# Kernel tuning notes

Hardware: AMD Instinct MI355X
Metric: run time of the kernel (lower is better)

## Reference

```python
import jax, jax.numpy as jnp
import numpy as np
from jax import lax

NEG = -1e30  # log-space 'zero' (avoid -inf for mixed-precision safety)
EPS = 1e-7   # keras backend epsilon used in ctc_batch_cost


def setup_inputs() -> dict:
    key = jax.random.key(0)
    k1, k2 = jax.random.split(key)
    B, T, L, V = 64, 1024, 128, 512
    # labels in [0, V-2]; blank index is V-1 (keras ctc_batch_cost convention)
    y_true = jax.random.randint(k1, (B, L), 0, V - 1, dtype=jnp.int64)
    # y_pred are softmax probabilities (ctc_batch_cost logs them internally)
    y_pred = jax.random.uniform(k2, (B, T, V), dtype=jnp.float32)
    y_pred = y_pred / jnp.sum(y_pred, axis=-1, keepdims=True)
    return {"y_true": y_true, "y_pred": y_pred}


def _ctc_loss(y_true, y_pred):
    # y_true: [B, L] int labels; y_pred: [B, T, V] probabilities
    B, T, V = y_pred.shape
    L = y_true.shape[1]
    blank = V - 1
    S = 2 * L + 1  # extended label length: blank,l1,blank,l2,...,blank

    logp = jnp.log(y_pred + EPS)  # [B, T, V]

    # extended label sequence per batch row
    ext = jnp.full((B, S), blank, dtype=y_true.dtype)
    ext = ext.at[:, 1::2].set(y_true)  # [B, S]

    # gather log-probs of extended labels at every time step -> [B, T, S]
    idx = jnp.broadcast_to(ext[:, None, :], (B, T, S))
    lp = jnp.take_along_axis(logp, idx, axis=2)

    # skip transition s-2 -> s allowed iff ext[s] != blank and ext[s] != ext[s-2]
    prev2 = jnp.concatenate([jnp.full((B, 2), -1, dtype=ext.dtype), ext[:, :-2]], axis=1)
    allow_skip = (ext != blank) & (ext != prev2)  # [B, S]

    # init alpha at t=0: only states 0 (blank) and 1 (first label) reachable
    alpha0 = jnp.full((B, S), NEG, dtype=logp.dtype)
    alpha0 = alpha0.at[:, 0].set(lp[:, 0, 0]).at[:, 1].set(lp[:, 0, 1])

    pad1 = jnp.full((B, 1), NEG, dtype=logp.dtype)
    pad2 = jnp.full((B, 2), NEG, dtype=logp.dtype)

    def step(alpha, lp_t):  # alpha, lp_t: [B, S]
        a1 = jnp.concatenate([pad1, alpha[:, :-1]], axis=1)
        a2 = jnp.concatenate([pad2, alpha[:, :-2]], axis=1)
        a2 = jnp.where(allow_skip, a2, NEG)
        new = jnp.logaddexp(jnp.logaddexp(alpha, a1), a2) + lp_t
        return new, None

    lp_rest = jnp.moveaxis(lp[:, 1:], 1, 0)  # [T-1, B, S], time-major for scan
    alpha_T, _ = lax.scan(step, alpha0, lp_rest)

    # total prob ends in last blank or last label
    log_p = jnp.logaddexp(alpha_T[:, -1], alpha_T[:, -2])  # [B]
    return -log_p[:, None]  # [B, 1] like keras ctc_batch_cost


def reference(y_true, y_pred):
    return _ctc_loss(y_true, y_pred)
```

## Files before the change

### kernel.cpp

```cpp
#include <hip/hip_runtime.h>
#include <hip/hip_bf16.h>
#include <cstdint>


#define CTC_B 64
#define CTC_T 1024
#define CTC_L 128
#define CTC_V 512
#define BLANK (CTC_V - 1)
#define EPSF 1e-7f
#define LN2F 0.69314718055994530942f

#define CHUNK 16
#define NBUF  4
#define NCH   (CTC_T / CHUNK)
#define BIASE 60

__device__ __forceinline__ void gld_lds16(const float* g, float* l) {
    __builtin_amdgcn_global_load_lds(
        (const __attribute__((address_space(1))) unsigned int*)g,
        (__attribute__((address_space(3))) unsigned int*)l,
        16, 0, 0);
}

template<int CTRL>
__device__ __forceinline__ float dpp_mov0(float v) {
    int r = __builtin_amdgcn_update_dpp(0, __float_as_int(v), CTRL, 0xf, 0xf, false);
    return __int_as_float(r);
}
template<int CTRL>
__device__ __forceinline__ float dpp_max(float v) {
    int r = __builtin_amdgcn_update_dpp(__float_as_int(v), __float_as_int(v),
                                        CTRL, 0xf, 0xf, false);
    return fmaxf(v, __int_as_float(r));
}

__global__ __launch_bounds__(256, 1)
void ctc_fwd_stream(const int* __restrict__ y_true,
                    const float* __restrict__ y_pred,
                    float* __restrict__ out) {
    __shared__ __align__(16) float rows[NBUF][CHUNK][CTC_V];

    const int b = blockIdx.x;
    const int tid = threadIdx.x;
    const int wave = tid >> 6;
    const int lane = tid & 63;
    const float* __restrict__ yb = y_pred + (size_t)b * CTC_T * CTC_V;

    if (wave != 0) {
        const int w = wave - 1;
#define ISSUE(c_) do {                                                     \
            const int t0_ = (c_) * CHUNK;                                  \
            float* bufb_ = &rows[(c_) & (NBUF - 1)][0][0];                 \
            for (int l_ = w; l_ < CHUNK; l_ += 3) {                        \
                const float* g_ = yb + (size_t)(t0_ + l_) * CTC_V + lane * 4; \
                float* d_ = bufb_ + l_ * CTC_V;                            \
                gld_lds16(g_, d_);                                         \
                gld_lds16(g_ + 256, d_ + 256);                             \
            }                                                              \
        } while (0)

        ISSUE(0); ISSUE(1); ISSUE(2);
        if (w == 0) asm volatile("s_waitcnt vmcnt(24)" ::: "memory");
        else        asm volatile("s_waitcnt vmcnt(20)" ::: "memory");
        __builtin_amdgcn_s_barrier();
        __builtin_amdgcn_sched_barrier(0);

        for (int c = 0; c < NCH; ++c) {
            if (c + 3 < NCH) ISSUE(c + 3);
            if (c <= NCH - 4) {
                if (w == 0) asm volatile("s_waitcnt vmcnt(24)" ::: "memory");
                else        asm volatile("s_waitcnt vmcnt(20)" ::: "memory");
            } else if (c == NCH - 3) {
                if (w == 0) asm volatile("s_waitcnt vmcnt(12)" ::: "memory");
                else        asm volatile("s_waitcnt vmcnt(10)" ::: "memory");
            } else if (c == NCH - 2) {
                asm volatile("s_waitcnt vmcnt(0)" ::: "memory");
            }
            __builtin_amdgcn_s_barrier();
            __builtin_amdgcn_sched_barrier(0);
        }
        return;
#undef ISSUE
    }

    const int labA = y_true[b * CTC_L + 2 * lane];
    const int labB = y_true[b * CTC_L + 2 * lane + 1];
    const int labPrev = __shfl_up(labB, 1);
    const float msk1 = (labA != labPrev) ? 1.0f : 0.0f;
    const float msk3 = (labB != labA) ? 1.0f : 0.0f;

    float a0 = 0.0f, a1 = 0.0f, a2 = 0.0f, a3 = 0.0f, a4 = 0.0f;
    float curScale = 1.0f;
    int curE = 0, Eacc = 0;

    float pAA0, pBA0, blA0, pAA1, pBA1, blA1, pAA2, pBA2, blA2, pAA3, pBA3, blA3;
    float pAB0, pBB0, blB0, pAB1, pBB1, blB1, pAB2, pBB2, blB2, pAB3, pBB3, blB3;
    float pAC0, pBC0, blC0, pAC1, pBC1, blC1, pAC2, pBC2, blC2, pAC3, pBC3, blC3;

#define LOADG(S, l_) do {                                                  \
        const float* r0_ = bufc + ((l_) + 0) * CTC_V;                      \
        const float* r1_ = bufc + ((l_) + 1) * CTC_V;                      \
        const float* r2_ = bufc + ((l_) + 2) * CTC_V;                      \
        const float* r3_ = bufc + ((l_) + 3) * CTC_V;                      \
        pA##S##0 = r0_[labA]; pB##S##0 = r0_[labB]; bl##S##0 = r0_[BLANK]; \
        pA##S##1 = r1_[labA]; pB##S##1 = r1_[labB]; bl##S##1 = r1_[BLANK]; \
        pA##S##2 = r2_[labA]; pB##S##2 = r2_[labB]; bl##S##2 = r2_[BLANK]; \
        pA##S##3 = r3_[labA]; pB##S##3 = r3_[labB]; bl##S##3 = r3_[BLANK]; \
    } while (0)

#define DOSTEP(S, k) do {                                                  \
        const float pb_ = bl##S##k + EPSF;                                 \
        const float pA_ = pA##S##k + EPSF;                                 \
        const float pB_ = pB##S##k + EPSF;                                 \
        const float pm1_ = dpp_mov0<0x138>(a3);  \
        const float n0_ = (a0 + pm1_) * pb_;                               \
        const float n1_ = fmaf(msk1, pm1_, a0 + a1) * pA_;                 \
        const float n2_ = (a1 + a2) * pb_;                                 \
        const float n3_ = fmaf(msk3, a1, a2 + a3) * pB_;                   \
        const float n4_ = (a3 + a4) * pb_;                                 \
        a0 = n0_; a1 = n1_; a2 = n2_; a3 = n3_; a4 = n4_;                  \
    } while (0)

#define DORN() do {                                                        \
        a0 *= curScale; a1 *= curScale; a2 *= curScale;                    \
        a3 *= curScale; a4 *= curScale;                                    \
        Eacc += curE;                                                      \
        float m_ = fmaxf(fmaxf(fmaxf(a0, a1), fmaxf(a2, a3)), a4);         \
        m_ = dpp_max<0x111>(m_);                           \
        m_ = dpp_max<0x112>(m_);                           \
        m_ = dpp_max<0x114>(m_);                           \
        m_ = dpp_max<0x118>(m_);                           \
        m_ = dpp_max<0x142>(m_);                         \
        m_ = dpp_max<0x143>(m_);                         \
        const int mb_ = __builtin_amdgcn_readlane(__float_as_int(m_), 63); \
        const int e_ = (mb_ >> 23) & 255;                                  \
        int k_ = 127 + BIASE + 127 - e_;                                   \
        k_ = k_ > 254 ? 254 : (k_ < 1 ? 1 : k_);                           \
        curScale = __int_as_float((unsigned)k_ << 23);                     \
        curE = 127 - k_;                                                   \
    } while (0)

#define PROC4_RN(S) do {                                                   \
        DOSTEP(S, 0); DORN();                                              \
        DOSTEP(S, 1); DOSTEP(S, 2); DOSTEP(S, 3);                          \
    } while (0)

    __builtin_amdgcn_s_barrier();
    __builtin_amdgcn_sched_barrier(0);

    for (int c = 0; c < NCH; ++c) {
        const float* bufc = &rows[c & (NBUF - 1)][0][0];
        if (c == 0) {
            const float pb0 = bufc[BLANK] + EPSF;
            const float plA = bufc[labA] + EPSF;
            LOADG(A, 0); LOADG(B, 4); LOADG(C, 8);
            a0 = (lane == 0) ? pb0 : 0.0f;
            a1 = (lane == 0) ? plA : 0.0f;
            DOSTEP(A, 1); DOSTEP(A, 2); DOSTEP(A, 3);
            LOADG(A, 12);
            PROC4_RN(B);
            PROC4_RN(C);
            PROC4_RN(A);
        } else {
            LOADG(A, 0); LOADG(B, 4); LOADG(C, 8);
            PROC4_RN(A); LOADG(A, 12);
            PROC4_RN(B); PROC4_RN(C); PROC4_RN(A);
        }
        __builtin_amdgcn_s_barrier();
        __builtin_amdgcn_sched_barrier(0);
    }

    if (lane == 63) {
        out[b] = -(logf(a3 + a4) + (float)Eacc * LN2F);
    }

#undef PROC4_RN
#undef DORN
#undef DOSTEP
#undef LOADG
}

extern "C" void kernel_launch(void* const* d_in, const int* in_sizes, int n_in,
                              void* d_out, int out_size, void* d_ws, size_t ws_size,
                              hipStream_t stream) {
    (void)in_sizes; (void)n_in; (void)d_ws; (void)ws_size; (void)out_size;
    const int* y_true = (const int*)d_in[0];
    const float* y_pred = (const float*)d_in[1];
    float* out = (float*)d_out;

    ctc_fwd_stream<<<CTC_B, 256, 0, stream>>>(y_true, y_pred, out);
}
```

Baseline: 71.42 us.

## Split CTC into parallel bf16 gather kernel plus compact serial scan kernel

Adds a gather kernel launched over 4096 blocks that reads the full probability tensor with all CUs. For each time step it keeps only the label and blank probabilities, packed as bf16 into a compact workspace of 68 words per row. A second kernel, one block per batch row, then runs the serial alpha recursion, streaming this small buffer through a deeper 8-slot LDS ring with a single loader wave. The goal is to lift the bandwidth limit of streaming the whole vocabulary through only 64 blocks, at the cost of an extra launch and bf16 rounding of the probabilities. The original single-kernel path is kept as a fallback when the workspace is too small.

```diff
diff --git a/kernel.cpp b/kernel.cpp
--- a/kernel.cpp
+++ b/kernel.cpp
@@ -11,16 +11,27 @@
 #define EPSF 1e-7f
 #define LN2F 0.69314718055994530942f
 
+#define ROWW 68
+#define K1ROWS 16
 #define CHUNK 16
-#define NBUF  4
+#define NBUF  8
 #define NCH   (CTC_T / CHUNK)
 #define BIASE 60
 
-__device__ __forceinline__ void gld_lds16(const float* g, float* l) {
+__device__ __forceinline__ void gld_lds16(const uint32_t* g, uint32_t* l) {
     __builtin_amdgcn_global_load_lds(
         (const __attribute__((address_space(1))) unsigned int*)g,
-        (__attribute__((address_space(3))) unsigned int*)l,
-        16, 0, 0);
+        (__attribute__((address_space(3))) unsigned int*)l, 16, 0, 0);
+}
+__device__ __forceinline__ void gld_lds4(const uint32_t* g, uint32_t* l) {
+    __builtin_amdgcn_global_load_lds(
+        (const __attribute__((address_space(1))) unsigned int*)g,
+        (__attribute__((address_space(3))) unsigned int*)l, 4, 0, 0);
+}
+__device__ __forceinline__ void gld_lds16f(const float* g, float* l) {
+    __builtin_amdgcn_global_load_lds(
+        (const __attribute__((address_space(1))) unsigned int*)g,
+        (__attribute__((address_space(3))) unsigned int*)l, 16, 0, 0);
 }
 
 template<int CTRL>
@@ -35,48 +46,81 @@
     return fmaxf(v, __int_as_float(r));
 }
 
+__device__ __forceinline__ uint32_t rne16(float x) {
+    return (__float_as_uint(x) + 0x8000u) >> 16;
+}
+
 __global__ __launch_bounds__(256, 1)
-void ctc_fwd_stream(const int* __restrict__ y_true,
-                    const float* __restrict__ y_pred,
-                    float* __restrict__ out) {
-    __shared__ __align__(16) float rows[NBUF][CHUNK][CTC_V];
+void ctc_gather(const int* __restrict__ y_true,
+                const float* __restrict__ y_pred,
+                uint32_t* __restrict__ cmp) {
+    __shared__ __align__(16) float rows[K1ROWS][CTC_V];
+
+    const int bid = blockIdx.x;
+    const int b = bid >> 6;
+    const int t0 = (bid & 63) * K1ROWS;
+    const int w = threadIdx.x >> 6;
+    const int lane = threadIdx.x & 63;
+    const float* __restrict__ yb = y_pred + ((size_t)b * CTC_T + t0) * CTC_V;
+
+    const int2 lp = *(const int2*)&y_true[b * CTC_L + 2 * lane];
+
+#pragma unroll
+    for (int r = 0; r < 4; ++r) {
+        const int row = 4 * w + r;
+        const float* g = yb + (size_t)row * CTC_V + lane * 4;
+        gld_lds16f(g, &rows[row][0]);
+        gld_lds16f(g + 256, &rows[row][256]);
+    }
+    asm volatile("s_waitcnt vmcnt(0)" ::: "memory");
+
+#pragma unroll
+    for (int r = 0; r < 4; ++r) {
+        const int row = 4 * w + r;
+        const float* rowp = &rows[row][0];
+        const float c0 = rowp[lp.x];
+        const float c1 = rowp[lp.y];
+        const uint32_t pk = rne16(c0) | (rne16(c1) << 16);
+        uint32_t* od = cmp + ((size_t)b * CTC_T + t0 + row) * ROWW;
+        od[lane] = pk;
+        if (lane == 63) od[64] = rne16(rowp[BLANK]);
+    }
+}
+
+__global__ __launch_bounds__(128, 1)
+void ctc_scan(const int* __restrict__ y_true,
+              const uint32_t* __restrict__ cmp,
+              float* __restrict__ out) {
+    __shared__ __align__(16) uint32_t ring[NBUF][CHUNK][ROWW];
 
     const int b = blockIdx.x;
-    const int tid = threadIdx.x;
-    const int wave = tid >> 6;
-    const int lane = tid & 63;
-    const float* __restrict__ yb = y_pred + (size_t)b * CTC_T * CTC_V;
-
-    if (wave != 0) {
-        const int w = wave - 1;
+    const int wave = threadIdx.x >> 6;
+    const int lane = threadIdx.x & 63;
+    const uint32_t* __restrict__ cb = cmp + (size_t)b * CTC_T * ROWW;
+
+    if (wave == 1) {
 #define ISSUE(c_) do {                                                     \
-            const int t0_ = (c_) * CHUNK;                                  \
-            float* bufb_ = &rows[(c_) & (NBUF - 1)][0][0];                 \
-            for (int l_ = w; l_ < CHUNK; l_ += 3) {                        \
-                const float* g_ = yb + (size_t)(t0_ + l_) * CTC_V + lane * 4; \
-                float* d_ = bufb_ + l_ * CTC_V;                            \
-                gld_lds16(g_, d_);                                         \
-                gld_lds16(g_ + 256, d_ + 256);                             \
-            }                                                              \
+            const uint32_t* g_ = cb + (size_t)(c_) * (CHUNK * ROWW);       \
+            uint32_t* d_ = &ring[(c_) & (NBUF - 1)][0][0];                 \
+            gld_lds16(g_ + lane * 4,        d_);                           \
+            gld_lds16(g_ + 256 + lane * 4,  d_ + 256);                     \
+            gld_lds16(g_ + 512 + lane * 4,  d_ + 512);                     \
+            gld_lds16(g_ + 768 + lane * 4,  d_ + 768);                     \
+            gld_lds4 (g_ + 1024 + lane,     d_ + 1024);                    \
         } while (0)
-
-        ISSUE(0); ISSUE(1); ISSUE(2);
-        if (w == 0) asm volatile("s_waitcnt vmcnt(24)" ::: "memory");
-        else        asm volatile("s_waitcnt vmcnt(20)" ::: "memory");
+        ISSUE(0); ISSUE(1); ISSUE(2); ISSUE(3); ISSUE(4); ISSUE(5);
+        asm volatile("s_waitcnt vmcnt(25)" ::: "memory");
         __builtin_amdgcn_s_barrier();
         __builtin_amdgcn_sched_barrier(0);
-
         for (int c = 0; c < NCH; ++c) {
-            if (c + 3 < NCH) ISSUE(c + 3);
-            if (c <= NCH - 4) {
-                if (w == 0) asm volatile("s_waitcnt vmcnt(24)" ::: "memory");
-                else        asm volatile("s_waitcnt vmcnt(20)" ::: "memory");
-            } else if (c == NCH - 3) {
-                if (w == 0) asm volatile("s_waitcnt vmcnt(12)" ::: "memory");
-                else        asm volatile("s_waitcnt vmcnt(10)" ::: "memory");
-            } else if (c == NCH - 2) {
-                asm volatile("s_waitcnt vmcnt(0)" ::: "memory");
-            }
+            if (c + 6 < NCH) ISSUE(c + 6);
+            const int K = (NCH - 1 - c < 6) ? (NCH - 1 - c) : 6;
+            if (K == 6)      asm volatile("s_waitcnt vmcnt(25)" ::: "memory");
+            else if (K == 5) asm volatile("s_waitcnt vmcnt(20)" ::: "memory");
+            else if (K == 4) asm volatile("s_waitcnt vmcnt(15)" ::: "memory");
+            else if (K == 3) asm volatile("s_waitcnt vmcnt(10)" ::: "memory");
+            else if (K == 2) asm volatile("s_waitcnt vmcnt(5)"  ::: "memory");
+            else if (K == 1) asm volatile("s_waitcnt vmcnt(0)"  ::: "memory");
             __builtin_amdgcn_s_barrier();
             __builtin_amdgcn_sched_barrier(0);
         }
@@ -94,25 +138,25 @@
     float curScale = 1.0f;
     int curE = 0, Eacc = 0;
 
-    float pAA0, pBA0, blA0, pAA1, pBA1, blA1, pAA2, pBA2, blA2, pAA3, pBA3, blA3;
-    float pAB0, pBB0, blB0, pAB1, pBB1, blB1, pAB2, pBB2, blB2, pAB3, pBB3, blB3;
-    float pAC0, pBC0, blC0, pAC1, pBC1, blC1, pAC2, pBC2, blC2, pAC3, pBC3, blC3;
+    uint32_t vA0, vA1, vA2, vA3, bA0, bA1, bA2, bA3;
+    uint32_t vB0, vB1, vB2, vB3, bB0, bB1, bB2, bB3;
+    uint32_t vC0, vC1, vC2, vC3, bC0, bC1, bC2, bC3;
 
 #define LOADG(S, l_) do {                                                  \
-        const float* r0_ = bufc + ((l_) + 0) * CTC_V;                      \
-        const float* r1_ = bufc + ((l_) + 1) * CTC_V;                      \
-        const float* r2_ = bufc + ((l_) + 2) * CTC_V;                      \
-        const float* r3_ = bufc + ((l_) + 3) * CTC_V;                      \
-        pA##S##0 = r0_[labA]; pB##S##0 = r0_[labB]; bl##S##0 = r0_[BLANK]; \
-        pA##S##1 = r1_[labA]; pB##S##1 = r1_[labB]; bl##S##1 = r1_[BLANK]; \
-        pA##S##2 = r2_[labA]; pB##S##2 = r2_[labB]; bl##S##2 = r2_[BLANK]; \
-        pA##S##3 = r3_[labA]; pB##S##3 = r3_[labB]; bl##S##3 = r3_[BLANK]; \
+        const uint32_t* r0_ = bufc + ((l_) + 0) * ROWW;                    \
+        const uint32_t* r1_ = bufc + ((l_) + 1) * ROWW;                    \
+        const uint32_t* r2_ = bufc + ((l_) + 2) * ROWW;                    \
+        const uint32_t* r3_ = bufc + ((l_) + 3) * ROWW;                    \
+        v##S##0 = r0_[lane]; b##S##0 = r0_[64];                            \
+        v##S##1 = r1_[lane]; b##S##1 = r1_[64];                            \
+        v##S##2 = r2_[lane]; b##S##2 = r2_[64];                            \
+        v##S##3 = r3_[lane]; b##S##3 = r3_[64];                            \
     } while (0)
 
 #define DOSTEP(S, k) do {                                                  \
-        const float pb_ = bl##S##k + EPSF;                                 \
-        const float pA_ = pA##S##k + EPSF;                                 \
-        const float pB_ = pB##S##k + EPSF;                                 \
+        const float pb_ = __uint_as_float(b##S##k << 16) + EPSF;           \
+        const float pA_ = __uint_as_float(v##S##k << 16) + EPSF;           \
+        const float pB_ = __uint_as_float(v##S##k & 0xffff0000u) + EPSF;   \
         const float pm1_ = dpp_mov0<0x138>(a3);  \
         const float n0_ = (a0 + pm1_) * pb_;                               \
         const float n1_ = fmaf(msk1, pm1_, a0 + a1) * pA_;                 \
@@ -150,13 +194,15 @@
     __builtin_amdgcn_sched_barrier(0);
 
     for (int c = 0; c < NCH; ++c) {
-        const float* bufc = &rows[c & (NBUF - 1)][0][0];
+        const uint32_t* bufc = &ring[c & (NBUF - 1)][0][0];
         if (c == 0) {
-            const float pb0 = bufc[BLANK] + EPSF;
-            const float plA = bufc[labA] + EPSF;
+            const uint32_t u0 = bufc[0];
+            const uint32_t ub0 = bufc[64];
             LOADG(A, 0); LOADG(B, 4); LOADG(C, 8);
+            const float pb0 = __uint_as_float(ub0 << 16) + EPSF;
+            const float pl0 = __uint_as_float(u0 << 16) + EPSF;
             a0 = (lane == 0) ? pb0 : 0.0f;
-            a1 = (lane == 0) ? plA : 0.0f;
+            a1 = (lane == 0) ? pl0 : 0.0f;
             DOSTEP(A, 1); DOSTEP(A, 2); DOSTEP(A, 3);
             LOADG(A, 12);
             PROC4_RN(B);
@@ -174,20 +220,161 @@
     if (lane == 63) {
         out[b] = -(logf(a3 + a4) + (float)Eacc * LN2F);
     }
-
 #undef PROC4_RN
 #undef DORN
 #undef DOSTEP
 #undef LOADG
 }
 
+#define F_CHUNK 16
+#define F_NBUF  4
+#define F_NCH   (CTC_T / F_CHUNK)
+
+__global__ __launch_bounds__(256, 1)
+void ctc_fwd_stream(const int* __restrict__ y_true,
+                    const float* __restrict__ y_pred,
+                    float* __restrict__ out) {
+    __shared__ __align__(16) float rows[F_NBUF][F_CHUNK][CTC_V];
+    const int b = blockIdx.x;
+    const int tid = threadIdx.x;
+    const int wave = tid >> 6;
+    const int lane = tid & 63;
+    const float* __restrict__ yb = y_pred + (size_t)b * CTC_T * CTC_V;
+
+    if (wave != 0) {
+        const int w = wave - 1;
+#define FISSUE(c_) do {                                                    \
+            const int t0_ = (c_) * F_CHUNK;                                \
+            float* bufb_ = &rows[(c_) & (F_NBUF - 1)][0][0];               \
+            for (int l_ = w; l_ < F_CHUNK; l_ += 3) {                      \
+                const float* g_ = yb + (size_t)(t0_ + l_) * CTC_V + lane * 4; \
+                float* d_ = bufb_ + l_ * CTC_V;                            \
+                gld_lds16f(g_, d_);                                        \
+                gld_lds16f(g_ + 256, d_ + 256);                            \
+            }                                                              \
+        } while (0)
+        FISSUE(0); FISSUE(1); FISSUE(2);
+        if (w == 0) asm volatile("s_waitcnt vmcnt(24)" ::: "memory");
+        else        asm volatile("s_waitcnt vmcnt(20)" ::: "memory");
+        __builtin_amdgcn_s_barrier();
+        __builtin_amdgcn_sched_barrier(0);
+        for (int c = 0; c < F_NCH; ++c) {
+            if (c + 3 < F_NCH) FISSUE(c + 3);
+            if (c <= F_NCH - 4) {
+                if (w == 0) asm volatile("s_waitcnt vmcnt(24)" ::: "memory");
+                else        asm volatile("s_waitcnt vmcnt(20)" ::: "memory");
+            } else if (c == F_NCH - 3) {
+                if (w == 0) asm volatile("s_waitcnt vmcnt(12)" ::: "memory");
+                else        asm volatile("s_waitcnt vmcnt(10)" ::: "memory");
+            } else if (c == F_NCH - 2) {
+                asm volatile("s_waitcnt vmcnt(0)" ::: "memory");
+            }
+            __builtin_amdgcn_s_barrier();
+            __builtin_amdgcn_sched_barrier(0);
+        }
+        return;
+#undef FISSUE
+    }
+
+    const int labA = y_true[b * CTC_L + 2 * lane];
+    const int labB = y_true[b * CTC_L + 2 * lane + 1];
+    const int labPrev = __shfl_up(labB, 1);
+    const float msk1 = (labA != labPrev) ? 1.0f : 0.0f;
+    const float msk3 = (labB != labA) ? 1.0f : 0.0f;
+
+    float a0 = 0.0f, a1 = 0.0f, a2 = 0.0f, a3 = 0.0f, a4 = 0.0f;
+    float curScale = 1.0f;
+    int curE = 0, Eacc = 0;
+    float pAA0, pBA0, blA0, pAA1, pBA1, blA1, pAA2, pBA2, blA2, pAA3, pBA3, blA3;
+    float pAB0, pBB0, blB0, pAB1, pBB1, blB1, pAB2, pBB2, blB2, pAB3, pBB3, blB3;
+    float pAC0, pBC0, blC0, pAC1, pBC1, blC1, pAC2, pBC2, blC2, pAC3, pBC3, blC3;
+
+#define FLOADG(S, l_) do {                                                 \
+        const float* r0_ = bufc + ((l_) + 0) * CTC_V;                      \
+        const float* r1_ = bufc + ((l_) + 1) * CTC_V;                      \
+        const float* r2_ = bufc + ((l_) + 2) * CTC_V;                      \
+        const float* r3_ = bufc + ((l_) + 3) * CTC_V;                      \
+        pA##S##0 = r0_[labA]; pB##S##0 = r0_[labB]; bl##S##0 = r0_[BLANK]; \
+        pA##S##1 = r1_[labA]; pB##S##1 = r1_[labB]; bl##S##1 = r1_[BLANK]; \
+        pA##S##2 = r2_[labA]; pB##S##2 = r2_[labB]; bl##S##2 = r2_[BLANK]; \
+        pA##S##3 = r3_[labA]; pB##S##3 = r3_[labB]; bl##S##3 = r3_[BLANK]; \
+    } while (0)
+#define FDOSTEP(S, k) do {                                                 \
+        const float pb_ = bl##S##k + EPSF;                                 \
+        const float pA_ = pA##S##k + EPSF;                                 \
+        const float pB_ = pB##S##k + EPSF;                                 \
+        const float pm1_ = dpp_mov0<0x138>(a3);                            \
+        const float n0_ = (a0 + pm1_) * pb_;                               \
+        const float n1_ = fmaf(msk1, pm1_, a0 + a1) * pA_;                 \
+        const float n2_ = (a1 + a2) * pb_;                                 \
+        const float n3_ = fmaf(msk3, a1, a2 + a3) * pB_;                   \
+        const float n4_ = (a3 + a4) * pb_;                                 \
+        a0 = n0_; a1 = n1_; a2 = n2_; a3 = n3_; a4 = n4_;                  \
+    } while (0)
+#define FDORN() do {                                                       \
+        a0 *= curScale; a1 *= curScale; a2 *= curScale;                    \
+        a3 *= curScale; a4 *= curScale;                                    \
+        Eacc += curE;                                                      \
+        float m_ = fmaxf(fmaxf(fmaxf(a0, a1), fmaxf(a2, a3)), a4);         \
+        m_ = dpp_max<0x111>(m_); m_ = dpp_max<0x112>(m_);                  \
+        m_ = dpp_max<0x114>(m_); m_ = dpp_max<0x118>(m_);                  \
+        m_ = dpp_max<0x142>(m_); m_ = dpp_max<0x143>(m_);                  \
+        const int mb_ = __builtin_amdgcn_readlane(__float_as_int(m_), 63); \
+        const int e_ = (mb_ >> 23) & 255;                                  \
+        int k_ = 127 + BIASE + 127 - e_;                                   \
+        k_ = k_ > 254 ? 254 : (k_ < 1 ? 1 : k_);                           \
+        curScale = __int_as_float((unsigned)k_ << 23);                     \
+        curE = 127 - k_;                                                   \
+    } while (0)
+#define FPROC4_RN(S) do {                                                  \
+        FDOSTEP(S, 0); FDORN();                                            \
+        FDOSTEP(S, 1); FDOSTEP(S, 2); FDOSTEP(S, 3);                       \
+    } while (0)
+
+    __builtin_amdgcn_s_barrier();
+    __builtin_amdgcn_sched_barrier(0);
+    for (int c = 0; c < F_NCH; ++c) {
+        const float* bufc = &rows[c & (F_NBUF - 1)][0][0];
+        if (c == 0) {
+            const float pb0 = bufc[BLANK] + EPSF;
+            const float plA = bufc[labA] + EPSF;
+            FLOADG(A, 0); FLOADG(B, 4); FLOADG(C, 8);
+            a0 = (lane == 0) ? pb0 : 0.0f;
+            a1 = (lane == 0) ? plA : 0.0f;
+            FDOSTEP(A, 1); FDOSTEP(A, 2); FDOSTEP(A, 3);
+            FLOADG(A, 12);
+            FPROC4_RN(B); FPROC4_RN(C); FPROC4_RN(A);
+        } else {
+            FLOADG(A, 0); FLOADG(B, 4); FLOADG(C, 8);
+            FPROC4_RN(A); FLOADG(A, 12);
+            FPROC4_RN(B); FPROC4_RN(C); FPROC4_RN(A);
+        }
+        __builtin_amdgcn_s_barrier();
+        __builtin_amdgcn_sched_barrier(0);
+    }
+    if (lane == 63) {
+        out[b] = -(logf(a3 + a4) + (float)Eacc * LN2F);
+    }
+#undef FPROC4_RN
+#undef FDORN
+#undef FDOSTEP
+#undef FLOADG
+}
+
 extern "C" void kernel_launch(void* const* d_in, const int* in_sizes, int n_in,
                               void* d_out, int out_size, void* d_ws, size_t ws_size,
                               hipStream_t stream) {
-    (void)in_sizes; (void)n_in; (void)d_ws; (void)ws_size; (void)out_size;
+    (void)in_sizes; (void)n_in; (void)out_size;
     const int* y_true = (const int*)d_in[0];
     const float* y_pred = (const float*)d_in[1];
     float* out = (float*)d_out;
 
-    ctc_fwd_stream<<<CTC_B, 256, 0, stream>>>(y_true, y_pred, out);
-}
+    const size_t need = (size_t)CTC_B * CTC_T * ROWW * sizeof(uint32_t);
+    if (ws_size >= need) {
+        uint32_t* cmp = (uint32_t*)d_ws;
+        ctc_gather<<<CTC_B * (CTC_T / K1ROWS), 256, 0, stream>>>(y_true, y_pred, cmp);
+        ctc_scan<<<CTC_B, 128, 0, stream>>>(y_true, cmp, out);
+    } else {
+        ctc_fwd_stream<<<CTC_B, 256, 0, stream>>>(y_true, y_pred, out);
+    }
+}
```

Result: slower. 91.47 us (+28.1%).
